# Kernel optimization log

Hardware: AMD Instinct MI355X
Metric: run time of the kernel (lower is better)

The kernel has to match this reference:

```python
import jax, jax.numpy as jnp
import numpy as np

BODY_EDGES = [(0, 2), (0, 5), (2, 7), (5, 8), (11, 12), (0, 11), (0, 12), (7, 11), (8, 12), (11, 13), (13, 15), (12, 14), (14, 16), (11, 23), (12, 24), (23, 24), (11, 24), (12, 23)]
N_JOINTS = 33
N_FEAT = 52
HIDDEN = 128
BN_EPS = 1e-5


def _make_adj():
    a = np.eye(N_JOINTS, dtype=np.float32)
    for i, j in BODY_EDGES:
        a[i, j] = 1.0
        a[j, i] = 1.0
    deg = np.clip(a.sum(1), 1.0, None)
    d = deg ** -0.5
    return jnp.asarray(d[:, None] * a * d[None, :])


def setup_inputs() -> dict:
    key = jax.random.key(0)
    ks = iter(jax.random.split(key, 40))
    B, T = 64, 256
    def lin(k, i, o):
        return jax.random.normal(k, (i, o), jnp.float32) / np.sqrt(i)
    inp = {
        'x': jax.random.normal(next(ks), (B, T, N_JOINTS, N_FEAT), jnp.float32),
        'adj': _make_adj(),
        # layer 0: in 52 -> out 128 (has skip linear)
        'W0': lin(next(ks), N_FEAT, HIDDEN), 'b0': jax.random.normal(next(ks), (HIDDEN,)) * 0.02,
        'S0': lin(next(ks), N_FEAT, HIDDEN), 'sb0': jax.random.normal(next(ks), (HIDDEN,)) * 0.02,
        'g0': 1.0 + 0.1 * jax.random.normal(next(ks), (HIDDEN,)), 'be0': 0.1 * jax.random.normal(next(ks), (HIDDEN,)),
        'm0': 0.1 * jax.random.normal(next(ks), (HIDDEN,)), 'v0': 1.0 + 0.1 * jax.random.uniform(next(ks), (HIDDEN,)),
        # layers 1,2: 128 -> 128 (identity skip)
        'W1': lin(next(ks), HIDDEN, HIDDEN), 'b1': jax.random.normal(next(ks), (HIDDEN,)) * 0.02,
        'g1': 1.0 + 0.1 * jax.random.normal(next(ks), (HIDDEN,)), 'be1': 0.1 * jax.random.normal(next(ks), (HIDDEN,)),
        'm1': 0.1 * jax.random.normal(next(ks), (HIDDEN,)), 'v1': 1.0 + 0.1 * jax.random.uniform(next(ks), (HIDDEN,)),
        'W2': lin(next(ks), HIDDEN, HIDDEN), 'b2': jax.random.normal(next(ks), (HIDDEN,)) * 0.02,
        'g2': 1.0 + 0.1 * jax.random.normal(next(ks), (HIDDEN,)), 'be2': 0.1 * jax.random.normal(next(ks), (HIDDEN,)),
        'm2': 0.1 * jax.random.normal(next(ks), (HIDDEN,)), 'v2': 1.0 + 0.1 * jax.random.uniform(next(ks), (HIDDEN,)),
        # temporal attention MLP: 128 -> 128 -> 1
        'tW1': lin(next(ks), HIDDEN, HIDDEN), 'tb1': jax.random.normal(next(ks), (HIDDEN,)) * 0.02,
        'tW2': lin(next(ks), HIDDEN, 1), 'tb2': jax.random.normal(next(ks), (1,)) * 0.02,
    }
    return inp


def _gcn(h, adj, W, b, g, be, m, v, skip):
    # adjacency mix: [B*T, J, D_in]
    a = jnp.einsum('nm,bmd->bnd', adj, h)
    z = a @ W + b
    z = (z - m) * jax.lax.rsqrt(v + BN_EPS) * g + be  # eval-mode BatchNorm1d
    return jax.nn.gelu(z, approximate=False) + skip


def reference(x, adj, W0, b0, S0, sb0, g0, be0, m0, v0,
              W1, b1, g1, be1, m1, v1,
              W2, b2, g2, be2, m2, v2,
              tW1, tb1, tW2, tb2):
    B, T, J, Fd = x.shape
    h = x.reshape(B * T, J, Fd)
    h = _gcn(h, adj, W0, b0, g0, be0, m0, v0, h @ S0 + sb0)
    h = _gcn(h, adj, W1, b1, g1, be1, m1, v1, h)
    h = _gcn(h, adj, W2, b2, g2, be2, m2, v2, h)
    # dropout inactive (eval mode)
    xt = h.mean(axis=1).reshape(B, T, -1)                  # [B, T, H]
    score = jax.nn.gelu(xt @ tW1 + tb1, approximate=False) @ tW2 + tb2  # [B, T, 1]
    attn = jax.nn.softmax(score, axis=1)
    return (xt * attn).sum(axis=1)                         # [B, H]
```

## Files before the change

### kernel.cpp

```cpp
#include <hip/hip_runtime.h>
#include <hip/hip_bf16.h>
#include <math.h>


#define NJ 33
#define NF 52
#define NH 128
#define NT 256
#define NB 64
#define NSAMP (NB*NT)
#define SPB 2
#define NBLKS (NSAMP/SPB)
#define HSTR 136
#define PSTR 40

typedef unsigned short u16;
typedef _Float16 f16;
typedef f16   half8 __attribute__((ext_vector_type(8)));
typedef f16   h2    __attribute__((ext_vector_type(2)));
typedef float f32x4 __attribute__((ext_vector_type(4)));

#define HO_W0    0
#define HO_S0    8192
#define HO_W1    16384
#define HO_W2    32768
#define HO_TW1   49152
#define HO_ADJ32 65536
#define H_TOTAL  66560
#define FO_BASE  (H_TOTAL/2)
#define FO_A0    (FO_BASE+0)
#define FO_SB0   (FO_BASE+768)
#define FO_TB1   (FO_BASE+896)
#define FO_TW2   (FO_BASE+1024)
#define FO_FLG   (FO_BASE+1152)
#define FO_XT    (FO_BASE+1280)
#define FO_SC    (FO_XT + NSAMP*NH)

__device__ __forceinline__ float bf2f(u16 u) { return __uint_as_float(((unsigned)u) << 16); }
__device__ __forceinline__ float ldv(const void* p, long i, int f) {
    float r;
    if (f) r = bf2f(((const u16*)p)[i]);
    else   r = ((const float*)p)[i];
    return r;
}
__device__ int detect_bf16(const void* p) {
    const u16* q = (const u16*)p;
    int nz = 0, ok = 0;
#pragma unroll
    for (int k = 0; k < 64; k++) {
        u16 u = q[k];
        if (u & 0x7FFF) {
            nz++;
            int e = (u >> 7) & 0xFF;
            ok += (e >= 0x40 && e <= 0xBF) ? 1 : 0;
        }
    }
    return (nz == 0) || (ok * 20 >= nz * 19);
}

__device__ __forceinline__ float gelu_c(float x) {
    float xc = fminf(fmaxf(x, -8.f), 8.f);
    float u  = xc * fmaf(xc * xc, 0.10294324f, 2.3022082f);
#if __has_builtin(__builtin_amdgcn_exp2f)
    float e  = __builtin_amdgcn_exp2f(u);
#else
    float e  = exp2f(u);
#endif
#if __has_builtin(__builtin_amdgcn_rcpf)
    float tt = (e - 1.f) * __builtin_amdgcn_rcpf(e + 1.f);
#else
    float tt = (e - 1.f) / (e + 1.f);
#endif
    float hx = 0.5f * x;
    return fmaf(hx, tt, hx);
}

#define MFMA16(a, b, c) __builtin_amdgcn_mfma_f32_16x16x32_f16(a, b, c, 0, 0, 0)

__global__ __launch_bounds__(256) void prep(
    const void* x, const void* adj,
    const void* W0, const void* b0, const void* S0, const void* sb0,
    const void* g0, const void* be0, const void* m0, const void* v0,
    const void* W1, const void* b1, const void* g1, const void* be1, const void* m1, const void* v1,
    const void* W2, const void* b2, const void* g2, const void* be2, const void* m2, const void* v2,
    const void* tW1, const void* tb1, const void* tW2,
    void* ws)
{
    f16* H = (f16*)ws; float* F = (float*)ws;
    const int bi = blockIdx.x, t = threadIdx.x;

    if (bi < 64) {
        const void* src; int dst, kt, nt, Kvalid, Kd;
        if (bi < 16)      { src = W1;  dst = HO_W1;  kt = (bi>>2)&3;    nt = bi&3;      Kvalid = 128; Kd = 128; }
        else if (bi < 32) { src = W2;  dst = HO_W2;  kt = ((bi-16)>>2); nt = (bi-16)&3; Kvalid = 128; Kd = 128; }
        else if (bi < 48) { src = tW1; dst = HO_TW1; kt = ((bi-32)>>2); nt = (bi-32)&3; Kvalid = 128; Kd = 128; }
        else if (bi < 56) { src = W0;  dst = HO_W0;  kt = ((bi-48)>>2); nt = (bi-48)&3; Kvalid = NF;  Kd = 64;  }
        else              { src = S0;  dst = HO_S0;  kt = ((bi-56)>>2); nt = (bi-56)&3; Kvalid = NF;  Kd = 64;  }
        const int flag = detect_bf16(src);
        __shared__ float tile[32][33];
        const int tx = t & 31, ty = t >> 5;
#pragma unroll
        for (int r = 0; r < 4; r++) {
            int k = kt*32 + ty + r*8;
            int n = nt*32 + tx;
            tile[ty + r*8][tx] = (k < Kvalid) ? ldv(src, (long)k*128 + n, flag) : 0.f;
        }
        __syncthreads();
#pragma unroll
        for (int r = 0; r < 4; r++) {
            int n = nt*32 + ty + r*8;
            int k = kt*32 + tx;
            H[dst + n*Kd + k] = (f16)tile[tx][ty + r*8];
        }
    } else {
        if (t == 0) ((int*)F)[FO_FLG] = detect_bf16(x);
        if (t < 128) {
            int c = t;
            {
                float g = ldv(g0,c,detect_bf16(g0)), be = ldv(be0,c,detect_bf16(be0));
                float m = ldv(m0,c,detect_bf16(m0)), v = ldv(v0,c,detect_bf16(v0));
                float b = ldv(b0,c,detect_bf16(b0));
                float A = g * rsqrtf(v + 1e-5f);
                F[FO_A0 + 0*256 + c] = A; F[FO_A0 + 0*256 + 128 + c] = (b - m)*A + be;
            }
            {
                float g = ldv(g1,c,detect_bf16(g1)), be = ldv(be1,c,detect_bf16(be1));
                float m = ldv(m1,c,detect_bf16(m1)), v = ldv(v1,c,detect_bf16(v1));
                float b = ldv(b1,c,detect_bf16(b1));
                float A = g * rsqrtf(v + 1e-5f);
                F[FO_A0 + 1*256 + c] = A; F[FO_A0 + 1*256 + 128 + c] = (b - m)*A + be;
            }
            {
                float g = ldv(g2,c,detect_bf16(g2)), be = ldv(be2,c,detect_bf16(be2));
                float m = ldv(m2,c,detect_bf16(m2)), v = ldv(v2,c,detect_bf16(v2));
                float b = ldv(b2,c,detect_bf16(b2));
                float A = g * rsqrtf(v + 1e-5f);
                F[FO_A0 + 2*256 + c] = A; F[FO_A0 + 2*256 + 128 + c] = (b - m)*A + be;
            }
            F[FO_SB0 + c] = ldv(sb0, c, detect_bf16(sb0));
            F[FO_TB1 + c] = ldv(tb1, c, detect_bf16(tb1));
            F[FO_TW2 + c] = ldv(tW2, c, detect_bf16(tW2));
        }
        const int fA = detect_bf16(adj);
        for (int i = t; i < 1024; i += 256) {
            int r = i >> 5, c = i & 31;
            float v = (r < 25 && c < 25) ? ldv(adj, (long)r*NJ + c, fA) : 0.f;
            H[HO_ADJ32 + i] = (f16)v;
        }
    }
}

#define PTWRITE(ACC)                                                            \
    _Pragma("unroll")                                                           \
    for (int mt = 0; mt < 4; mt++) {                                            \
        const int fF = mt >> 1;                                                 \
        const int jb = (mt & 1) * 16;                                           \
        _Pragma("unroll")                                                       \
        for (int nt = 0; nt < 2; nt++) {                                        \
            f16* pp = Pt + (fF*128 + (nt ? c1 : c0))*PSTR;                      \
            _Pragma("unroll")                                                   \
            for (int r2 = 0; r2 < 4; r2 += 2) {                                 \
                int j0 = jb + q*4 + r2;                                         \
                if (j0 + 1 < 25) {                                              \
                    h2 v2w = { (f16)ACC[mt][nt][r2], (f16)ACC[mt][nt][r2+1] };  \
                    *(h2*)(pp + j0) = v2w;                                      \
                } else if (j0 < 25) {                                           \
                    pp[j0] = (f16)ACC[mt][nt][r2];                              \
                }                                                               \
            }                                                                   \
        }                                                                       \
    }

#define ADJEPI(L, WRHB) {                                                       \
    f32x4 zac[2][2][2];                                                         \
    _Pragma("unroll")                                                           \
    for (int fF = 0; fF < 2; fF++) {                                            \
        _Pragma("unroll")                                                       \
        for (int nt = 0; nt < 2; nt++) {                                        \
            half8 bz = *(const half8*)(Pt + (fF*128 + (nt?c1:c0))*PSTR + q*8);  \
            zac[fF][0][nt] = MFMA16(afadj0, bz, z4);                            \
            zac[fF][1][nt] = MFMA16(afadj1, bz, z4);                            \
        }                                                                       \
    }                                                                           \
    _Pragma("unroll")                                                           \
    for (int nt = 0; nt < 2; nt++) {                                            \
        const int cc = nt ? c1 : c0;                                            \
        const float Av = rA[L][nt], Dv = rD[L][nt];                             \
        _Pragma("unroll")                                                       \
        for (int fF = 0; fF < 2; fF++) {                                        \
            _Pragma("unroll")                                                   \
            for (int m2 = 0; m2 < 2; m2++) {                                    \
                _Pragma("unroll")                                               \
                for (int r4 = 0; r4 < 4; r4++) {                                \
                    float zv = (m2 == 0) ? zac[fF][0][nt][r4]                   \
                             : (jlt[r4] ? zac[fF][1][nt][r4]                    \
                                        : acc[2*fF+1][nt][r4]);                 \
                    float hnew = gelu_c(fmaf(zv, Av, Dv)) + hz[fF][m2][nt][r4]; \
                    hz[fF][m2][nt][r4] = hnew;                                  \
                    if (WRHB)                                                   \
                        hb[((2*fF+m2)*16 + q*4 + r4)*HSTR + cc] = (f16)hnew;    \
                }                                                               \
            }                                                                   \
            {                                                                   \
                float hnew = gelu_c(fmaf(acc[4][nt][fF], Av, Dv)) + h32[fF][nt];\
                h32[fF][nt] = (q == 0) ? hnew : 0.f;                            \
                if (WRHB && q == 0)                                             \
                    hb[(64 + fF)*HSTR + cc] = (f16)hnew;                        \
            }                                                                   \
        }                                                                       \
    }                                                                           \
}

#define GEMM128(WOFF)                                                           \
    {                                                                           \
        half8 bf[2][4];                                                         \
        _Pragma("unroll")                                                       \
        for (int nt = 0; nt < 2; nt++)                                          \
            _Pragma("unroll")                                                   \
            for (int ks = 0; ks < 4; ks++)                                      \
                bf[nt][ks] = *(const half8*)(HW + (WOFF) + (nt?c1:c0)*128 + ks*32 + q*8); \
        _Pragma("unroll")                                                       \
        for (int mt = 0; mt < 5; mt++) { acc[mt][0] = z4; acc[mt][1] = z4; }    \
        _Pragma("unroll")                                                       \
        for (int mt = 0; mt < 5; mt++) {                                        \
            const int m = mt*16 + ml;                                           \
            _Pragma("unroll")                                                   \
            for (int ks = 0; ks < 4; ks++) {                                    \
                half8 af = *(const half8*)(hb + m*HSTR + ks*32 + q*8);          \
                acc[mt][0] = MFMA16(af, bf[0][ks], acc[mt][0]);                 \
                acc[mt][1] = MFMA16(af, bf[1][ks], acc[mt][1]);                 \
            }                                                                   \
        }                                                                       \
    }

__global__ __launch_bounds__(256) void gcn_mfma(const void* __restrict__ x,
                                                void* __restrict__ ws)
{
    __shared__ __align__(16) f16 hb[80 * HSTR];
    __shared__ __align__(16) f16 Pt[2 * 128 * PSTR];
    __shared__ float rbuf4[4];
    float* xtb = (float*)Pt;

    const f16* HW = (const f16*)ws;
    float* F = (float*)ws;
    float* xt_g = F + FO_XT;
    float* sc_g = F + FO_SC;
    const int t = threadIdx.x, lane = t & 63, wv = t >> 6;
    const int q = lane >> 4, ml = lane & 15;
    const int n0 = wv * 32;
    const int c0 = n0 + ml, c1 = n0 + 16 + ml;
    const f32x4 z4 = {0.f, 0.f, 0.f, 0.f};
    const bool jlt[4] = { q <= 2, q <= 1, q <= 1, q <= 1 };
    const half8 zero8 = {(f16)0.f,(f16)0.f,(f16)0.f,(f16)0.f,(f16)0.f,(f16)0.f,(f16)0.f,(f16)0.f};
#pragma unroll
    for (int i = t; i < 512; i += 256) {
        int fF = i >> 8, rem = i & 255, n = rem >> 1, chh = rem & 1;
        *(half8*)(Pt + (fF*128 + n)*PSTR + 24 + chh*8) = zero8;
    }
    float rA[3][2], rD[3][2];
#pragma unroll
    for (int L = 0; L < 3; L++) {
        rA[L][0] = F[FO_A0 + L*256 + c0];        rA[L][1] = F[FO_A0 + L*256 + c1];
        rD[L][0] = F[FO_A0 + L*256 + 128 + c0];  rD[L][1] = F[FO_A0 + L*256 + 128 + c1];
    }
    const float sb0a = F[FO_SB0 + c0], sb0b = F[FO_SB0 + c1];
    half8 afadj0 = *(const half8*)(HW + HO_ADJ32 + ml*32 + q*8);
    half8 afadj1 = *(const half8*)(HW + HO_ADJ32 + (16+ml)*32 + q*8);
    __syncthreads();
    {
        const int fX = ((const int*)F)[FO_FLG];
        const long xb = (long)blockIdx.x * (SPB * NJ * NF);
#pragma unroll 1
        for (int it = 0; it < 3; it++) {
            int g = t + it * 256;
            if (g < 66 * 8) {
                int r = g >> 3, blk = g & 7;
                int fF = (r >= 33) ? 1 : 0;
                int j = r - 33 * fF;
                int fr = (j < 32) ? (fF * 32 + j) : (64 + fF);
                half8 o;
                if (!fX) {
                    const float* base = (const float*)x + xb + (long)r * NF + blk * 8;
                    if (blk < 6) {
                        float4 v0 = *(const float4*)base;
                        float4 v1 = *(const float4*)(base + 4);
                        o[0]=(f16)v0.x; o[1]=(f16)v0.y; o[2]=(f16)v0.z; o[3]=(f16)v0.w;
                        o[4]=(f16)v1.x; o[5]=(f16)v1.y; o[6]=(f16)v1.z; o[7]=(f16)v1.w;
                    } else if (blk == 6) {
                        float4 v0 = *(const float4*)base;
                        o = zero8;
                        o[0]=(f16)v0.x; o[1]=(f16)v0.y; o[2]=(f16)v0.z; o[3]=(f16)v0.w;
                    } else o = zero8;
                } else {
                    long rb = xb + (long)r * NF;
#pragma unroll
                    for (int i = 0; i < 8; i++) {
                        int cx = blk * 8 + i;
                        o[i] = (f16)(cx < NF ? bf2f(((const u16*)x)[rb + cx]) : 0.f);
                    }
                }
                *(half8*)(hb + fr * HSTR + blk * 8) = o;
            }
        }
    }
    __syncthreads();
    f32x4 acc[5][2];
    float hz[2][2][2][4];
    float h32[2][2];
    {
        half8 bw[2][2], bs[2][2];
#pragma unroll
        for (int nt = 0; nt < 2; nt++) {
            int n = nt ? c1 : c0;
#pragma unroll
            for (int ks = 0; ks < 2; ks++) {
                bw[nt][ks] = *(const half8*)(HW + HO_W0 + n*64 + ks*32 + q*8);
                bs[nt][ks] = *(const half8*)(HW + HO_S0 + n*64 + ks*32 + q*8);
            }
        }
        f32x4 acs[5][2];
#pragma unroll
        for (int mt = 0; mt < 5; mt++) { acc[mt][0]=z4; acc[mt][1]=z4; acs[mt][0]=z4; acs[mt][1]=z4; }
#pragma unroll
        for (int mt = 0; mt < 5; mt++) {
            const int m = mt*16 + ml;
            half8 a0 = *(const half8*)(hb + m*HSTR + q*8);
            half8 a1 = *(const half8*)(hb + m*HSTR + 32 + q*8);
            acc[mt][0] = MFMA16(a0, bw[0][0], acc[mt][0]);
            acc[mt][0] = MFMA16(a1, bw[0][1], acc[mt][0]);
            acc[mt][1] = MFMA16(a0, bw[1][0], acc[mt][1]);
            acc[mt][1] = MFMA16(a1, bw[1][1], acc[mt][1]);
            acs[mt][0] = MFMA16(a0, bs[0][0], acs[mt][0]);
            acs[mt][0] = MFMA16(a1, bs[0][1], acs[mt][0]);
            acs[mt][1] = MFMA16(a0, bs[1][0], acs[mt][1]);
            acs[mt][1] = MFMA16(a1, bs[1][1], acs[mt][1]);
        }
        __syncthreads();
        PTWRITE(acc)
#pragma unroll
        for (int fF = 0; fF < 2; fF++)
#pragma unroll
            for (int m2 = 0; m2 < 2; m2++)
#pragma unroll
                for (int nt = 0; nt < 2; nt++)
#pragma unroll
                    for (int r4 = 0; r4 < 4; r4++)
                        hz[fF][m2][nt][r4] = acs[2*fF+m2][nt][r4] + (nt ? sb0b : sb0a);
#pragma unroll
        for (int fF = 0; fF < 2; fF++)
#pragma unroll
            for (int nt = 0; nt < 2; nt++)
                h32[fF][nt] = (q == 0) ? (acs[4][nt][fF] + (nt ? sb0b : sb0a)) : 0.f;
        ADJEPI(0, 1)
        __syncthreads();
    }
    GEMM128(HO_W1)
    __syncthreads();
    PTWRITE(acc)
    ADJEPI(1, 1)
    __syncthreads();
    GEMM128(HO_W2)
    __syncthreads();
    PTWRITE(acc)
    ADJEPI(2, 0)
    __syncthreads();
#pragma unroll
    for (int fF = 0; fF < 2; fF++)
#pragma unroll
        for (int nt = 0; nt < 2; nt++) {
            float s = h32[fF][nt];
#pragma unroll
            for (int m2 = 0; m2 < 2; m2++)
#pragma unroll
                for (int r4 = 0; r4 < 4; r4++) s += hz[fF][m2][nt][r4];
            s += __shfl_xor(s, 16, 64);
            s += __shfl_xor(s, 32, 64);
            float xtc = s * (1.0f / 33.0f);
            if (q == 0) {
                int cc = nt ? c1 : c0;
                xtb[fF * 128 + cc] = xtc;
                xt_g[((long)blockIdx.x * SPB + fF) * NH + cc] = xtc;
            }
        }
    __syncthreads();
    {
        const int fF = t >> 7, c = t & 127;
        float u = 0.f;
#pragma unroll
        for (int kk = 0; kk < 16; kk++) {
            half8 wv8 = *(const half8*)(HW + HO_TW1 + c*128 + kk*8);
#pragma unroll
            for (int i = 0; i < 8; i++)
                u = fmaf(xtb[fF*128 + kk*8 + i], (float)wv8[i], u);
        }
        float r = gelu_c(u + F[FO_TB1 + c]) * F[FO_TW2 + c];
#pragma unroll
        for (int off = 32; off > 0; off >>= 1) r += __shfl_xor(r, off, 64);
        if (lane == 0) rbuf4[wv] = r;
        __syncthreads();
        if (t == 0) {
            sc_g[blockIdx.x * SPB + 0] = rbuf4[0] + rbuf4[1];
            sc_g[blockIdx.x * SPB + 1] = rbuf4[2] + rbuf4[3];
        }
    }
}

__global__ __launch_bounds__(256) void attn_pool(
    const int* __restrict__ flg,
    const float* __restrict__ xt_ws, const float* __restrict__ score_ws,
    void* __restrict__ out)
{
    __shared__ float ew[NT];
    __shared__ float red[8];
    __shared__ float pb[256];
    const int t = threadIdx.x, lane = t & 63, wv = t >> 6;
    const int b = blockIdx.x >> 2, qr = blockIdx.x & 3;

    float sv = score_ws[b * NT + t];
    float m = sv;
#pragma unroll
    for (int off = 32; off > 0; off >>= 1) m = fmaxf(m, __shfl_xor(m, off, 64));
    if (lane == 0) red[wv] = m;
    __syncthreads();
    float mx = fmaxf(fmaxf(red[0], red[1]), fmaxf(red[2], red[3]));
    float e = __expf(sv - mx);
    ew[t] = e;
    float d = e;
#pragma unroll
    for (int off = 32; off > 0; off >>= 1) d += __shfl_xor(d, off, 64);
    if (lane == 0) red[4 + wv] = d;
    __syncthreads();
    float den = red[4] + red[5] + red[6] + red[7];

    const int cl = t & 31, ch = t >> 5;
    const int c = qr * 32 + cl;
    float a = 0.f;
#pragma unroll 4
    for (int i = ch * 32; i < ch * 32 + 32; i++)
        a = fmaf(ew[i], xt_ws[((long)b * NT + i) * NH + c], a);
    pb[t] = a;
    __syncthreads();
    if (t < 128) pb[t] += pb[t + 128];
    __syncthreads();
    if (t < 64) pb[t] += pb[t + 64];
    __syncthreads();
    if (t < 32) {
        float r = (pb[t] + pb[t + 32]) / den;
        if (*flg) ((__hip_bfloat16*)out)[b * NH + qr * 32 + t] = __float2bfloat16(r);
        else      ((float*)out)[b * NH + qr * 32 + t] = r;
    }
}

extern "C" void kernel_launch(void* const* d_in, const int* in_sizes, int n_in,
                              void* d_out, int out_size, void* d_ws, size_t ws_size,
                              hipStream_t stream) {
    prep<<<65, 256, 0, stream>>>(
        d_in[0], d_in[1],
        d_in[2], d_in[3], d_in[4], d_in[5],
        d_in[6], d_in[7], d_in[8], d_in[9],
        d_in[10], d_in[11], d_in[12], d_in[13], d_in[14], d_in[15],
        d_in[16], d_in[17], d_in[18], d_in[19], d_in[20], d_in[21],
        d_in[22], d_in[23], d_in[24],
        d_ws);
    gcn_mfma<<<NBLKS, 256, 0, stream>>>(d_in[0], d_ws);
    float* F = (float*)d_ws;
    attn_pool<<<NB * 4, 256, 0, stream>>>((const int*)(F + FO_FLG), F + FO_XT, F + FO_SC, d_out);
}
```

Measured before the change: 537.7 us.

## Add 512-thread GCN kernel variant with one 16-column tile per wave

Adds a gcn_mfma_w kernel that uses 8 waves per block, each owning 16 output channels instead of 32, which halves the per-wave accumulator and weight-fragment state. At launch time it checks the compiled register count and scratch usage and picks the wide variant only if it fits in 128 VGPRs without spilling, otherwise it falls back to the original 256-thread kernel. The aim is more waves in flight for better latency hiding, at the cost of more redundant LDS A-fragment reads and larger blocks.

```diff
diff --git a/kernel.cpp b/kernel.cpp
--- a/kernel.cpp
+++ b/kernel.cpp
@@ -233,8 +233,8 @@
         }                                                                       \
     }
 
-__global__ __launch_bounds__(256) void gcn_mfma(const void* __restrict__ x,
-                                                void* __restrict__ ws)
+__global__ __launch_bounds__(256) void gcn_mfma_a(const void* __restrict__ x,
+                                                  void* __restrict__ ws)
 {
     __shared__ __align__(16) f16 hb[80 * HSTR];
     __shared__ __align__(16) f16 Pt[2 * 128 * PSTR];
@@ -405,6 +405,258 @@
     }
 }
 
+__global__ __launch_bounds__(512) void gcn_mfma_w(const void* __restrict__ x,
+                                                  void* __restrict__ ws)
+{
+    __shared__ __align__(16) f16 hb[80 * HSTR];
+    __shared__ __align__(16) f16 Pt[2 * 128 * PSTR];
+    __shared__ float rbuf4[4];
+    float* xtb = (float*)Pt;
+
+    const f16* HW = (const f16*)ws;
+    float* F = (float*)ws;
+    float* xt_g = F + FO_XT;
+    float* sc_g = F + FO_SC;
+    const int t = threadIdx.x, lane = t & 63, wv = t >> 6;
+    const int q = lane >> 4, ml = lane & 15;
+    const int c = wv * 16 + ml;
+    const f32x4 z4 = {0.f, 0.f, 0.f, 0.f};
+    const bool jlt[4] = { q <= 2, q <= 1, q <= 1, q <= 1 };
+    const half8 zero8 = {(f16)0.f,(f16)0.f,(f16)0.f,(f16)0.f,(f16)0.f,(f16)0.f,(f16)0.f,(f16)0.f};
+
+    {
+        int fF = t >> 8, rem = t & 255, n = rem >> 1, chh = rem & 1;
+        *(half8*)(Pt + (fF*128 + n)*PSTR + 24 + chh*8) = zero8;
+    }
+
+    float rA[3], rD[3];
+#pragma unroll
+    for (int L = 0; L < 3; L++) {
+        rA[L] = F[FO_A0 + L*256 + c];
+        rD[L] = F[FO_A0 + L*256 + 128 + c];
+    }
+    const float sb0v = F[FO_SB0 + c];
+    half8 afadj0 = *(const half8*)(HW + HO_ADJ32 + ml*32 + q*8);
+    half8 afadj1 = *(const half8*)(HW + HO_ADJ32 + (16+ml)*32 + q*8);
+    __syncthreads();
+
+    {
+        const int fX = ((const int*)F)[FO_FLG];
+        const long xb = (long)blockIdx.x * (SPB * NJ * NF);
+#pragma unroll 1
+        for (int it = 0; it < 2; it++) {
+            int g = t + it * 512;
+            if (g < 66 * 8) {
+                int r = g >> 3, blk = g & 7;
+                int fF = (r >= 33) ? 1 : 0;
+                int j = r - 33 * fF;
+                int fr = (j < 32) ? (fF * 32 + j) : (64 + fF);
+                half8 o;
+                if (!fX) {
+                    const float* base = (const float*)x + xb + (long)r * NF + blk * 8;
+                    if (blk < 6) {
+                        float4 v0 = *(const float4*)base;
+                        float4 v1 = *(const float4*)(base + 4);
+                        o[0]=(f16)v0.x; o[1]=(f16)v0.y; o[2]=(f16)v0.z; o[3]=(f16)v0.w;
+                        o[4]=(f16)v1.x; o[5]=(f16)v1.y; o[6]=(f16)v1.z; o[7]=(f16)v1.w;
+                    } else if (blk == 6) {
+                        float4 v0 = *(const float4*)base;
+                        o = zero8;
+                        o[0]=(f16)v0.x; o[1]=(f16)v0.y; o[2]=(f16)v0.z; o[3]=(f16)v0.w;
+                    } else o = zero8;
+                } else {
+                    long rb = xb + (long)r * NF;
+#pragma unroll
+                    for (int i = 0; i < 8; i++) {
+                        int cx = blk * 8 + i;
+                        o[i] = (f16)(cx < NF ? bf2f(((const u16*)x)[rb + cx]) : 0.f);
+                    }
+                }
+                *(half8*)(hb + fr * HSTR + blk * 8) = o;
+            }
+        }
+    }
+    __syncthreads();
+
+    f32x4 acc[5];
+    float hz[2][2][4];
+    float h32[2];
+
+    {
+        half8 bw[2], bs[2];
+#pragma unroll
+        for (int ks = 0; ks < 2; ks++) {
+            bw[ks] = *(const half8*)(HW + HO_W0 + c*64 + ks*32 + q*8);
+            bs[ks] = *(const half8*)(HW + HO_S0 + c*64 + ks*32 + q*8);
+        }
+        f32x4 acs[5];
+#pragma unroll
+        for (int mt = 0; mt < 5; mt++) { acc[mt] = z4; acs[mt] = z4; }
+#pragma unroll
+        for (int mt = 0; mt < 5; mt++) {
+            const int m = mt*16 + ml;
+            half8 a0 = *(const half8*)(hb + m*HSTR + q*8);
+            half8 a1 = *(const half8*)(hb + m*HSTR + 32 + q*8);
+            acc[mt] = MFMA16(a0, bw[0], acc[mt]);
+            acc[mt] = MFMA16(a1, bw[1], acc[mt]);
+            acs[mt] = MFMA16(a0, bs[0], acs[mt]);
+            acs[mt] = MFMA16(a1, bs[1], acs[mt]);
+        }
+        __syncthreads();
+#pragma unroll
+        for (int mt = 0; mt < 4; mt++) {
+            const int fF = mt >> 1;
+            const int jb = (mt & 1) * 16;
+            f16* pp = Pt + (fF*128 + c)*PSTR;
+#pragma unroll
+            for (int r2 = 0; r2 < 4; r2 += 2) {
+                int j0 = jb + q*4 + r2;
+                if (j0 + 1 < 25) {
+                    h2 v2w = { (f16)acc[mt][r2], (f16)acc[mt][r2+1] };
+                    *(h2*)(pp + j0) = v2w;
+                } else if (j0 < 25) {
+                    pp[j0] = (f16)acc[mt][r2];
+                }
+            }
+        }
+#pragma unroll
+        for (int fF = 0; fF < 2; fF++)
+#pragma unroll
+            for (int m2 = 0; m2 < 2; m2++)
+#pragma unroll
+                for (int r4 = 0; r4 < 4; r4++)
+                    hz[fF][m2][r4] = acs[2*fF+m2][r4] + sb0v;
+#pragma unroll
+        for (int fF = 0; fF < 2; fF++)
+            h32[fF] = (q == 0) ? (acs[4][fF] + sb0v) : 0.f;
+    }
+
+#define ADJEPI_W(L, WRHB) {                                                     \
+    f32x4 zac[2][2];                                                            \
+    _Pragma("unroll")                                                           \
+    for (int fF = 0; fF < 2; fF++) {                                            \
+        half8 bz = *(const half8*)(Pt + (fF*128 + c)*PSTR + q*8);               \
+        zac[fF][0] = MFMA16(afadj0, bz, z4);                                    \
+        zac[fF][1] = MFMA16(afadj1, bz, z4);                                    \
+    }                                                                           \
+    const float Av = rA[L], Dv = rD[L];                                         \
+    _Pragma("unroll")                                                           \
+    for (int fF = 0; fF < 2; fF++) {                                            \
+        _Pragma("unroll")                                                       \
+        for (int m2 = 0; m2 < 2; m2++) {                                        \
+            _Pragma("unroll")                                                   \
+            for (int r4 = 0; r4 < 4; r4++) {                                    \
+                float zv = (m2 == 0) ? zac[fF][0][r4]                           \
+                         : (jlt[r4] ? zac[fF][1][r4] : acc[2*fF+1][r4]);        \
+                float hnew = gelu_c(fmaf(zv, Av, Dv)) + hz[fF][m2][r4];         \
+                hz[fF][m2][r4] = hnew;                                          \
+                if (WRHB)                                                       \
+                    hb[((2*fF+m2)*16 + q*4 + r4)*HSTR + c] = (f16)hnew;         \
+            }                                                                   \
+        }                                                                       \
+        {                                                                       \
+            float hnew = gelu_c(fmaf(acc[4][fF], Av, Dv)) + h32[fF];            \
+            h32[fF] = (q == 0) ? hnew : 0.f;                                    \
+            if (WRHB && q == 0)                                                 \
+                hb[(64 + fF)*HSTR + c] = (f16)hnew;                             \
+        }                                                                       \
+    }                                                                           \
+}
+
+#define PTWRITE_W(ACC)                                                          \
+    _Pragma("unroll")                                                           \
+    for (int mt = 0; mt < 4; mt++) {                                            \
+        const int fF = mt >> 1;                                                 \
+        const int jb = (mt & 1) * 16;                                           \
+        f16* pp = Pt + (fF*128 + c)*PSTR;                                       \
+        _Pragma("unroll")                                                       \
+        for (int r2 = 0; r2 < 4; r2 += 2) {                                     \
+            int j0 = jb + q*4 + r2;                                             \
+            if (j0 + 1 < 25) {                                                  \
+                h2 v2w = { (f16)ACC[mt][r2], (f16)ACC[mt][r2+1] };              \
+                *(h2*)(pp + j0) = v2w;                                          \
+            } else if (j0 < 25) {                                               \
+                pp[j0] = (f16)ACC[mt][r2];                                      \
+            }                                                                   \
+        }                                                                       \
+    }
+
+#define GEMM128_W(WOFF)                                                         \
+    {                                                                           \
+        half8 bf[4];                                                            \
+        _Pragma("unroll")                                                       \
+        for (int ks = 0; ks < 4; ks++)                                          \
+            bf[ks] = *(const half8*)(HW + (WOFF) + c*128 + ks*32 + q*8);        \
+        _Pragma("unroll")                                                       \
+        for (int mt = 0; mt < 5; mt++) acc[mt] = z4;                            \
+        _Pragma("unroll")                                                       \
+        for (int mt = 0; mt < 5; mt++) {                                        \
+            const int m = mt*16 + ml;                                           \
+            _Pragma("unroll")                                                   \
+            for (int ks = 0; ks < 4; ks++) {                                    \
+                half8 af = *(const half8*)(hb + m*HSTR + ks*32 + q*8);          \
+                acc[mt] = MFMA16(af, bf[ks], acc[mt]);                          \
+            }                                                                   \
+        }                                                                       \
+    }
+
+    ADJEPI_W(0, 1)
+    __syncthreads();
+
+    GEMM128_W(HO_W1)
+    __syncthreads();
+    PTWRITE_W(acc)
+    ADJEPI_W(1, 1)
+    __syncthreads();
+
+    GEMM128_W(HO_W2)
+    __syncthreads();
+    PTWRITE_W(acc)
+    ADJEPI_W(2, 0)
+    __syncthreads();
+
+#pragma unroll
+    for (int fF = 0; fF < 2; fF++) {
+        float s = h32[fF];
+#pragma unroll
+        for (int m2 = 0; m2 < 2; m2++)
+#pragma unroll
+            for (int r4 = 0; r4 < 4; r4++) s += hz[fF][m2][r4];
+        s += __shfl_xor(s, 16, 64);
+        s += __shfl_xor(s, 32, 64);
+        float xtc = s * (1.0f / 33.0f);
+        if (q == 0) {
+            xtb[fF * 128 + c] = xtc;
+            xt_g[((long)blockIdx.x * SPB + fF) * NH + c] = xtc;
+        }
+    }
+    __syncthreads();
+
+    {
+        float r = 0.f;
+        if (t < 256) {
+            const int fF = t >> 7, ch = t & 127;
+            float u = 0.f;
+#pragma unroll
+            for (int kk = 0; kk < 16; kk++) {
+                half8 wv8 = *(const half8*)(HW + HO_TW1 + ch*128 + kk*8);
+#pragma unroll
+                for (int i = 0; i < 8; i++)
+                    u = fmaf(xtb[fF*128 + kk*8 + i], (float)wv8[i], u);
+            }
+            r = gelu_c(u + F[FO_TB1 + ch]) * F[FO_TW2 + ch];
+        }
+#pragma unroll
+        for (int off = 32; off > 0; off >>= 1) r += __shfl_xor(r, off, 64);
+        if (lane == 0 && wv < 4) rbuf4[wv] = r;
+        __syncthreads();
+        if (t == 0) {
+            sc_g[blockIdx.x * SPB + 0] = rbuf4[0] + rbuf4[1];
+            sc_g[blockIdx.x * SPB + 1] = rbuf4[2] + rbuf4[3];
+        }
+    }
+}
+
 __global__ __launch_bounds__(256) void attn_pool(
     const int* __restrict__ flg,
     const float* __restrict__ xt_ws, const float* __restrict__ score_ws,
@@ -454,6 +706,15 @@
 extern "C" void kernel_launch(void* const* d_in, const int* in_sizes, int n_in,
                               void* d_out, int out_size, void* d_ws, size_t ws_size,
                               hipStream_t stream) {
+    static int use_w = -1;
+    if (use_w < 0) {
+        hipFuncAttributes a{};
+        use_w = 0;
+        if (hipFuncGetAttributes(&a, reinterpret_cast<const void*>(gcn_mfma_w)) == hipSuccess
+            && a.numRegs > 0 && a.numRegs <= 128
+            && a.localSizeBytes == 0)
+            use_w = 1;
+    }
     prep<<<65, 256, 0, stream>>>(
         d_in[0], d_in[1],
         d_in[2], d_in[3], d_in[4], d_in[5],
@@ -462,7 +723,8 @@
         d_in[16], d_in[17], d_in[18], d_in[19], d_in[20], d_in[21],
         d_in[22], d_in[23], d_in[24],
         d_ws);
-    gcn_mfma<<<NBLKS, 256, 0, stream>>>(d_in[0], d_ws);
+    if (use_w) gcn_mfma_w<<<NBLKS, 512, 0, stream>>>(d_in[0], d_ws);
+    else       gcn_mfma_a<<<NBLKS, 256, 0, stream>>>(d_in[0], d_ws);
     float* F = (float*)d_ws;
     attn_pool<<<NB * 4, 256, 0, stream>>>((const int*)(F + FO_FLG), F + FO_XT, F + FO_SC, d_out);
 }
```

Result: faster. 511.3 us (-4.9%).
